# Optimization experiments

Measured on AMD Instinct MI355X. Metric: run time of the kernel, lower is better.

Reference implementation:

```python
import jax, jax.numpy as jnp
import numpy as np

N = 32768      # total nodes (2048 graphs * 16 nodes)
E = 491520     # total edges (2048 graphs * 16*15)
F = 11         # in_node_nf
H = 64         # hidden_nf
G = 2048       # number of graphs
NN = 16        # nodes per graph
R = 1024       # n_reactions
L = 4          # n_layers
EIN = 2 * H + 1        # edge_mlp input: [h[row], h[col], radial]
NIN = H + H + F        # node_mlp input: [h, agg, node_attr=h0]


def setup_inputs() -> dict:
    key = jax.random.key(0)
    ks = jax.random.split(key, 24)
    s = 0.05
    d = {
        "h0": jax.random.normal(ks[0], (N, F), jnp.float32),
        "positions": jax.random.normal(ks[1], (N, 3), jnp.float32),
        "edges": jax.random.randint(ks[2], (2, E), 0, N),
        "node_mask": jnp.ones((N, 1), jnp.float32),
        "edge_mask": jnp.ones((E, 1), jnp.float32),
        "reaction_indexes": jax.random.randint(ks[3], (G,), 0, R),
        "reaction_signs": jax.random.normal(ks[4], (G,), jnp.float32),
        # params
        "emb_w": jax.random.normal(ks[5], (F, H), jnp.float32) * s,
        "emb_b": jnp.zeros((H,), jnp.float32),
        "edge_w1": jax.random.normal(ks[6], (L, EIN, H), jnp.float32) * s,
        "edge_b1": jnp.zeros((L, H), jnp.float32),
        "edge_w2": jax.random.normal(ks[7], (L, H, H), jnp.float32) * s,
        "edge_b2": jnp.zeros((L, H), jnp.float32),
        "node_w1": jax.random.normal(ks[8], (L, NIN, H), jnp.float32) * s,
        "node_b1": jnp.zeros((L, H), jnp.float32),
        "node_w2": jax.random.normal(ks[9], (L, H, H), jnp.float32) * s,
        "node_b2": jnp.zeros((L, H), jnp.float32),
        "dec_w1": jax.random.normal(ks[10], (H, H), jnp.float32) * s,
        "dec_b1": jnp.zeros((H,), jnp.float32),
        "dec_w2": jax.random.normal(ks[11], (H, H), jnp.float32) * s,
        "dec_b2": jnp.zeros((H,), jnp.float32),
        "g_w1": jax.random.normal(ks[12], (H, H), jnp.float32) * s,
        "g_b1": jnp.zeros((H,), jnp.float32),
        "g_w2": jax.random.normal(ks[13], (H, 1), jnp.float32) * s,
        "g_b2": jnp.zeros((1,), jnp.float32),
        "n_nodes": NN,
        "n_reactions": R,
    }
    return d


def reference(h0, positions, edges, node_mask, edge_mask, reaction_indexes,
              reaction_signs, emb_w, emb_b, edge_w1, edge_b1, edge_w2, edge_b2,
              node_w1, node_b1, node_w2, node_b2, dec_w1, dec_b1, dec_w2,
              dec_b2, g_w1, g_b1, g_w2, g_b2, n_nodes, n_reactions):
    silu = jax.nn.silu
    row, col = edges[0], edges[1]
    n = h0.shape[0]

    # radial is constant across layers (coords never updated in this variant)
    coord_diff = positions[row] - positions[col]          # [E, 3]
    radial = jnp.sum(coord_diff ** 2, axis=1, keepdims=True)  # [E, 1]

    h = h0 @ emb_w + emb_b                                # [N, H]
    for i in range(edge_w1.shape[0]):
        # edge model
        e_in = jnp.concatenate([h[row], h[col], radial], axis=1)  # [E, 2H+1]
        e = silu(e_in @ edge_w1[i] + edge_b1[i])
        e = silu(e @ edge_w2[i] + edge_b2[i])             # [E, H]
        e = e * edge_mask
        # scatter-sum aggregation by source node
        agg = jax.ops.segment_sum(e, row, num_segments=n)  # [N, H]
        # node model (node_attr = h0)
        n_in = jnp.concatenate([h, agg, h0], axis=1)      # [N, 2H+F]
        h = silu(n_in @ node_w1[i] + node_b1[i]) @ node_w2[i] + node_b2[i]

    # node decoder
    h = silu(h @ dec_w1 + dec_b1) @ dec_w2 + dec_b2
    h = h * node_mask
    # pool per graph (fixed n_nodes per graph)
    hg = h.reshape(-1, n_nodes, h.shape[-1]).sum(axis=1)  # [G, H]
    # graph decoder
    temp = silu(hg @ g_w1 + g_b1) @ g_w2 + g_b2           # [G, 1]
    # signed per-reaction aggregation
    pred = jnp.zeros((n_reactions,), h.dtype).at[reaction_indexes].add(
        temp[:, 0] * reaction_signs)
    return pred
```

## Files before the change

kernel.cpp:

```cpp
#include <hip/hip_runtime.h>
#include <math.h>

#define N_NODES 32768
#define N_EDGES 491520
#define F_IN    11
#define H       64
#define G_GRAPHS 2048
#define NN_PER_G 16
#define R_REACT 1024
#define L_LAYERS 4
#define EIN     129
#define NIN     139
#define NPBLK   32

typedef __attribute__((ext_vector_type(8))) short short8;
typedef __attribute__((ext_vector_type(4))) float f32x4;

__device__ __forceinline__ float silu_f(float x) {
    return x * __builtin_amdgcn_rcpf(1.0f + __expf(-x));
}
__device__ __forceinline__ void atomAddF(float* p, float v) {
    unsafeAtomicAdd(p, v);
}
__device__ __forceinline__ float bf2f(unsigned short b) {
    union { float f; unsigned u; } v; v.u = ((unsigned)b) << 16;
    return v.f;
}
__device__ __forceinline__ unsigned short f2bf(float x) {
    union { float f; unsigned u; } v; v.f = x;
    unsigned r = v.u + 0x7FFFu + ((v.u >> 16) & 1u);
    return (unsigned short)(r >> 16);
}
__device__ __forceinline__ void splitbf(float x, unsigned short& hi, unsigned short& lo) {
    hi = f2bf(x);
    lo = f2bf(x - bf2f(hi));
}
__device__ __forceinline__ void splitbf_t(float x, unsigned short& hi, unsigned short& lo) {
    union { float f; unsigned u; } v; v.f = x;
    hi = (unsigned short)(v.u >> 16);
    union { float f; unsigned u; } w; w.f = x - bf2f(hi);
    lo = (unsigned short)(w.u >> 16);
}

__global__ __launch_bounds__(256) void k_embed(
        const float* __restrict__ h0, const float* __restrict__ emb_w,
        const float* __restrict__ emb_b, float* __restrict__ h,
        int* __restrict__ deg) {
    int tid = blockIdx.x * 256 + threadIdx.x;
    if (blockIdx.x < N_NODES / 256) deg[tid] = 0;
    int n = tid >> 6, j = tid & 63;
    float acc = emb_b[j];
#pragma unroll
    for (int k = 0; k < F_IN; ++k)
        acc += h0[n * F_IN + k] * emb_w[k * H + j];
    h[tid] = acc;
}

__global__ __launch_bounds__(256) void k_radial(
        const int* __restrict__ edges, const float* __restrict__ pos,
        float* __restrict__ radial) {
    int e = blockIdx.x * 256 + threadIdx.x;
    int r = edges[e], c = edges[N_EDGES + e];
    float dx = pos[r * 3 + 0] - pos[c * 3 + 0];
    float dy = pos[r * 3 + 1] - pos[c * 3 + 1];
    float dz = pos[r * 3 + 2] - pos[c * 3 + 2];
    radial[e] = dx * dx + dy * dy + dz * dz;
}

__global__ __launch_bounds__(256) void k_hist(
        const int* __restrict__ edges, int* __restrict__ deg) {
    int e = blockIdx.x * 256 + threadIdx.x;
    atomicAdd(&deg[edges[e]], 1);
}

__global__ __launch_bounds__(1024) void k_scan(
        const int* __restrict__ deg, int* __restrict__ nstart,
        int* __restrict__ cursor) {
    const int tid = threadIdx.x;
    const int lane = tid & 63, wv = tid >> 6;
    __shared__ int wsum[16];

    const int base = tid * 32;
    int local[32];
    int s = 0;
#pragma unroll
    for (int i = 0; i < 32; ++i) { local[i] = s; s += deg[base + i]; }

    int v = s;
#pragma unroll
    for (int off = 1; off < 64; off <<= 1) {
        int u = __shfl_up(v, off);
        if (lane >= off) v += u;
    }
    if (lane == 63) wsum[wv] = v;
    const int excl = v - s;
    __syncthreads();
    if (wv == 0 && lane < 16) {
        int w = wsum[lane];
        int vv = w;
#pragma unroll
        for (int off = 1; off < 16; off <<= 1) {
            int u = __shfl_up(vv, off);
            if (lane >= off) vv += u;
        }
        wsum[lane] = vv - w;
    }
    __syncthreads();
    const int bs = wsum[wv] + excl;
#pragma unroll
    for (int i = 0; i < 32; ++i) {
        int ns = bs + local[i];
        nstart[base + i] = ns;
        cursor[base + i] = ns;
    }
    if (tid == 0) nstart[N_NODES] = N_EDGES;
}

__global__ __launch_bounds__(256) void k_fill(
        const int* __restrict__ edges, const float* __restrict__ radial,
        const float* __restrict__ emask, int* __restrict__ cursor,
        int* __restrict__ csrP, float* __restrict__ csrR,
        float* __restrict__ csrM) {
    int e = blockIdx.x * 256 + threadIdx.x;
    int r = edges[e];
    int pos = atomicAdd(&cursor[r], 1);
    csrP[pos] = edges[N_EDGES + e] | ((r & (NPBLK - 1)) << 16);
    csrR[pos] = radial[e];
    csrM[pos] = emask[e];
}

__global__ __launch_bounds__(64, 1) void k_nodeproj_m(
        const float* __restrict__ h, const float* __restrict__ W1,
        const float* __restrict__ b1,
        float* __restrict__ PA, float* __restrict__ PB) {
    const int lane = threadIdx.x;
    const int quad = lane >> 4, m16 = lane & 15;

    short8 Bh[16], Bl[16];
#pragma unroll
    for (int nt = 0; nt < 8; ++nt) {
#pragma unroll
        for (int kf = 0; kf < 2; ++kf) {
            short8 bh, bl;
#pragma unroll
            for (int j = 0; j < 8; ++j) {
                int row = (nt >= 4 ? 64 : 0) + kf * 32 + quad * 8 + j;
                float w = W1[row * H + (nt & 3) * 16 + m16];
                unsigned short hi, lo; splitbf(w, hi, lo);
                bh[j] = (short)hi; bl[j] = (short)lo;
            }
            Bh[nt * 2 + kf] = bh; Bl[nt * 2 + kf] = bl;
        }
    }
    float b1v[4];
#pragma unroll
    for (int nt = 0; nt < 4; ++nt) b1v[nt] = b1[nt * 16 + m16];

    for (int t = 0; t < 2; ++t) {
        const int nb = (blockIdx.x * 2 + t) * 16;
        const float* hp = h + (nb + m16) * H + quad * 8;
        float av[16];
        *(float4*)&av[0]  = *(const float4*)(hp + 0);
        *(float4*)&av[4]  = *(const float4*)(hp + 4);
        *(float4*)&av[8]  = *(const float4*)(hp + 32);
        *(float4*)&av[12] = *(const float4*)(hp + 36);
        short8 Ah0, Ah1, Al0, Al1;
#pragma unroll
        for (int j = 0; j < 8; ++j) {
            unsigned short hi, lo;
            splitbf_t(av[j], hi, lo);     Ah0[j] = (short)hi; Al0[j] = (short)lo;
            splitbf_t(av[8 + j], hi, lo); Ah1[j] = (short)hi; Al1[j] = (short)lo;
        }
        f32x4 acc[8];
#pragma unroll
        for (int nt = 0; nt < 8; ++nt) {
            f32x4 a = {0.0f, 0.0f, 0.0f, 0.0f};
            a = __builtin_amdgcn_mfma_f32_16x16x32_bf16(Ah0, Bh[nt*2+0], a, 0, 0, 0);
            a = __builtin_amdgcn_mfma_f32_16x16x32_bf16(Ah1, Bh[nt*2+1], a, 0, 0, 0);
            a = __builtin_amdgcn_mfma_f32_16x16x32_bf16(Ah0, Bl[nt*2+0], a, 0, 0, 0);
            a = __builtin_amdgcn_mfma_f32_16x16x32_bf16(Ah1, Bl[nt*2+1], a, 0, 0, 0);
            a = __builtin_amdgcn_mfma_f32_16x16x32_bf16(Al0, Bh[nt*2+0], a, 0, 0, 0);
            a = __builtin_amdgcn_mfma_f32_16x16x32_bf16(Al1, Bh[nt*2+1], a, 0, 0, 0);
            acc[nt] = a;
        }
#pragma unroll
        for (int r4 = 0; r4 < 4; ++r4) {
            const int node = nb + quad * 4 + r4;
#pragma unroll
            for (int nt = 0; nt < 4; ++nt)
                PA[node * H + nt * 16 + m16] = acc[nt][r4] + b1v[nt];
#pragma unroll
            for (int nt = 4; nt < 8; ++nt)
                PB[node * H + (nt - 4) * 16 + m16] = acc[nt][r4];
        }
    }
}

__global__ __launch_bounds__(256, 2) void k_edge6(
        const float* __restrict__ PA, const float* __restrict__ PB,
        const int* __restrict__ nstart, const int* __restrict__ csrP,
        const float* __restrict__ csrR, const float* __restrict__ csrM,
        const float* __restrict__ W1,
        const float* __restrict__ W2, const float* __restrict__ b2,
        float* __restrict__ agg) {
    const int tid = threadIdx.x;
    const int lane = tid & 63, wave = tid >> 6;
    const int quad = lane >> 4, m16 = lane & 15;
    const int n0 = blockIdx.x * NPBLK;

    __shared__ float aggld[NPBLK * 68];
    for (int i = tid; i < NPBLK * 68; i += 256) aggld[i] = 0.0f;

    short8 Bh[8], Bl[8];
#pragma unroll
    for (int nt = 0; nt < 4; ++nt) {
#pragma unroll
        for (int kf = 0; kf < 2; ++kf) {
            short8 bh, bl;
#pragma unroll
            for (int j = 0; j < 8; ++j) {
                float w = W2[(kf * 32 + quad * 8 + j) * H + nt * 16 + m16];
                unsigned short hi, lo; splitbf(w, hi, lo);
                bh[j] = (short)hi; bl[j] = (short)lo;
            }
            Bh[nt * 2 + kf] = bh; Bl[nt * 2 + kf] = bl;
        }
    }
    float w1cr[16];
#pragma unroll
    for (int i = 0; i < 16; ++i) {
        int k = (i < 8) ? (quad * 8 + i) : (32 + quad * 8 + (i - 8));
        w1cr[i] = W1[128 * H + k];
    }
    float b2v[4];
#pragma unroll
    for (int nt = 0; nt < 4; ++nt) b2v[nt] = b2[nt * 16 + m16];

    const int start = nstart[n0];
    const int end   = nstart[n0 + NPBLK];
    __syncthreads();

    const int ntiles = (end - start + 15) >> 4;

    float radA = 0.0f, avA[16], bvA[16];
    int rlA = 0;
    int rlqA[4]; float mkqA[4];

    int t = wave;
    bool haveA = t < ntiles;
    if (haveA) {
        const int idx = start + t * 16 + m16;
        const int ss = min(idx, N_EDGES - 1);
        const int pk = csrP[ss];
        radA = csrR[ss];
        const int c = pk & 0xFFFF;
        rlA = pk >> 16;
        const int sb = start + t * 16 + quad * 4;
#pragma unroll
        for (int r4 = 0; r4 < 4; ++r4) {
            int s = sb + r4, s2 = min(s, N_EDGES - 1);
            rlqA[r4] = csrP[s2] >> 16;
            mkqA[r4] = (s < end) ? csrM[s2] : 0.0f;
        }
        const float* par = PA + (n0 + rlA) * H + quad * 8;
        const float* pbr = PB + c * H + quad * 8;
        *(float4*)&avA[0]  = *(const float4*)(par + 0);
        *(float4*)&avA[4]  = *(const float4*)(par + 4);
        *(float4*)&avA[8]  = *(const float4*)(par + 32);
        *(float4*)&avA[12] = *(const float4*)(par + 36);
        *(float4*)&bvA[0]  = *(const float4*)(pbr + 0);
        *(float4*)&bvA[4]  = *(const float4*)(pbr + 4);
        *(float4*)&bvA[8]  = *(const float4*)(pbr + 32);
        *(float4*)&bvA[12] = *(const float4*)(pbr + 36);
    }

    while (haveA) {
        const int tn = t + 4;
        const bool haveB = tn < ntiles;
        float radB = 0.0f, bvB[16];
        int rlB = 0;
        int rlqB[4]; float mkqB[4];
        if (haveB) {
            const int idx = start + tn * 16 + m16;
            const int ss = min(idx, N_EDGES - 1);
            const int pk = csrP[ss];
            radB = csrR[ss];
            const int c = pk & 0xFFFF;
            rlB = pk >> 16;
            const int sb = start + tn * 16 + quad * 4;
#pragma unroll
            for (int r4 = 0; r4 < 4; ++r4) {
                int s = sb + r4, s2 = min(s, N_EDGES - 1);
                rlqB[r4] = csrP[s2] >> 16;
                mkqB[r4] = (s < end) ? csrM[s2] : 0.0f;
            }
            const float* pbr = PB + c * H + quad * 8;
            *(float4*)&bvB[0]  = *(const float4*)(pbr + 0);
            *(float4*)&bvB[4]  = *(const float4*)(pbr + 4);
            *(float4*)&bvB[8]  = *(const float4*)(pbr + 32);
            *(float4*)&bvB[12] = *(const float4*)(pbr + 36);
        }

        short8 Ah0, Ah1, Al0, Al1;
#pragma unroll
        for (int i = 0; i < 8; ++i) {
            unsigned short hi, lo;
            splitbf_t(silu_f(avA[i] + bvA[i] + radA * w1cr[i]), hi, lo);
            Ah0[i] = (short)hi; Al0[i] = (short)lo;
            splitbf_t(silu_f(avA[8+i] + bvA[8+i] + radA * w1cr[8+i]), hi, lo);
            Ah1[i] = (short)hi; Al1[i] = (short)lo;
        }
        f32x4 acc[4];
#pragma unroll
        for (int nt = 0; nt < 4; ++nt) {
            f32x4 a = {0.0f, 0.0f, 0.0f, 0.0f};
            a = __builtin_amdgcn_mfma_f32_16x16x32_bf16(Ah0, Bh[nt*2+0], a, 0, 0, 0);
            a = __builtin_amdgcn_mfma_f32_16x16x32_bf16(Ah1, Bh[nt*2+1], a, 0, 0, 0);
            a = __builtin_amdgcn_mfma_f32_16x16x32_bf16(Ah0, Bl[nt*2+0], a, 0, 0, 0);
            a = __builtin_amdgcn_mfma_f32_16x16x32_bf16(Ah1, Bl[nt*2+1], a, 0, 0, 0);
            a = __builtin_amdgcn_mfma_f32_16x16x32_bf16(Al0, Bh[nt*2+0], a, 0, 0, 0);
            a = __builtin_amdgcn_mfma_f32_16x16x32_bf16(Al1, Bh[nt*2+1], a, 0, 0, 0);
            acc[nt] = a;
        }

#pragma unroll
        for (int nt = 0; nt < 4; ++nt) {
            float oo[4];
#pragma unroll
            for (int r4 = 0; r4 < 4; ++r4)
                oo[r4] = silu_f(acc[nt][r4] + b2v[nt]) * mkqA[r4];
            int cur = rlqA[0]; float s = oo[0];
#pragma unroll
            for (int r4 = 1; r4 < 4; ++r4) {
                if (rlqA[r4] == cur) { s += oo[r4]; }
                else {
                    atomicAdd(&aggld[cur * 68 + nt * 16 + m16], s);
                    cur = rlqA[r4]; s = oo[r4];
                }
            }
            atomicAdd(&aggld[cur * 68 + nt * 16 + m16], s);
        }

        if (haveB) {
            radA = radB; rlA = rlB;
#pragma unroll
            for (int r4 = 0; r4 < 4; ++r4) { rlqA[r4] = rlqB[r4]; mkqA[r4] = mkqB[r4]; }
            const float* par = PA + (n0 + rlA) * H + quad * 8;
            *(float4*)&avA[0]  = *(const float4*)(par + 0);
            *(float4*)&avA[4]  = *(const float4*)(par + 4);
            *(float4*)&avA[8]  = *(const float4*)(par + 32);
            *(float4*)&avA[12] = *(const float4*)(par + 36);
#pragma unroll
            for (int i = 0; i < 16; ++i) bvA[i] = bvB[i];
        }
        t = tn; haveA = haveB;
    }

    __syncthreads();
#pragma unroll
    for (int i = tid; i < NPBLK * 16; i += 256) {
        int n = i >> 4, cb = (i & 15) << 2;
        *(float4*)&agg[(n0 + n) * H + cb] = *(const float4*)&aggld[n * 68 + cb];
    }
}

__global__ __launch_bounds__(64, 1) void k_node_m(
        float* __restrict__ h, const float* __restrict__ agg,
        const float* __restrict__ h0,
        const float* __restrict__ W1, const float* __restrict__ b1,
        const float* __restrict__ W2, const float* __restrict__ b2) {
    const int lane = threadIdx.x;
    const int quad = lane >> 4, m16 = lane & 15;

    short8 B1h[20], B1l[20];
#pragma unroll
    for (int nt = 0; nt < 4; ++nt) {
#pragma unroll
        for (int kf = 0; kf < 5; ++kf) {
            short8 bh, bl;
#pragma unroll
            for (int j = 0; j < 8; ++j) {
                int row = kf * 32 + quad * 8 + j;
                float w = (row < NIN) ? W1[row * H + nt * 16 + m16] : 0.0f;
                unsigned short hi, lo; splitbf(w, hi, lo);
                bh[j] = (short)hi; bl[j] = (short)lo;
            }
            B1h[nt * 5 + kf] = bh; B1l[nt * 5 + kf] = bl;
        }
    }
    short8 B2h[8], B2l[8];
#pragma unroll
    for (int nt = 0; nt < 4; ++nt) {
#pragma unroll
        for (int kf = 0; kf < 2; ++kf) {
            short8 bh, bl;
#pragma unroll
            for (int j = 0; j < 8; ++j) {
                float w = W2[(kf * 32 + quad * 8 + j) * H + nt * 16 + m16];
                unsigned short hi, lo; splitbf(w, hi, lo);
                bh[j] = (short)hi; bl[j] = (short)lo;
            }
            B2h[nt * 2 + kf] = bh; B2l[nt * 2 + kf] = bl;
        }
    }
    float b1v[4], b2v[4];
#pragma unroll
    for (int nt = 0; nt < 4; ++nt) {
        b1v[nt] = b1[nt * 16 + m16];
        b2v[nt] = b2[nt * 16 + m16];
    }

    __shared__ float tld[16 * 68];

    for (int t = 0; t < 2; ++t) {
        const int nb = (blockIdx.x * 2 + t) * 16;
        float a1[5][8];
        const float* hp = h + (nb + m16) * H + quad * 8;
        const float* ap = agg + (nb + m16) * H + quad * 8;
        *(float4*)&a1[0][0] = *(const float4*)(hp + 0);
        *(float4*)&a1[0][4] = *(const float4*)(hp + 4);
        *(float4*)&a1[1][0] = *(const float4*)(hp + 32);
        *(float4*)&a1[1][4] = *(const float4*)(hp + 36);
        *(float4*)&a1[2][0] = *(const float4*)(ap + 0);
        *(float4*)&a1[2][4] = *(const float4*)(ap + 4);
        *(float4*)&a1[3][0] = *(const float4*)(ap + 32);
        *(float4*)&a1[3][4] = *(const float4*)(ap + 36);
        const float* h0p = h0 + (nb + m16) * F_IN;
#pragma unroll
        for (int j = 0; j < 8; ++j) {
            int kk = quad * 8 + j;
            a1[4][j] = (kk < F_IN) ? h0p[kk] : 0.0f;
        }
        short8 A1h[5], A1l[5];
#pragma unroll
        for (int kf = 0; kf < 5; ++kf) {
            short8 ah, al;
#pragma unroll
            for (int j = 0; j < 8; ++j) {
                unsigned short hi, lo; splitbf_t(a1[kf][j], hi, lo);
                ah[j] = (short)hi; al[j] = (short)lo;
            }
            A1h[kf] = ah; A1l[kf] = al;
        }
        f32x4 acc[4];
#pragma unroll
        for (int nt = 0; nt < 4; ++nt) {
            f32x4 a = {0.0f, 0.0f, 0.0f, 0.0f};
#pragma unroll
            for (int kf = 0; kf < 5; ++kf)
                a = __builtin_amdgcn_mfma_f32_16x16x32_bf16(A1h[kf], B1h[nt*5+kf], a, 0, 0, 0);
#pragma unroll
            for (int kf = 0; kf < 5; ++kf)
                a = __builtin_amdgcn_mfma_f32_16x16x32_bf16(A1l[kf], B1h[nt*5+kf], a, 0, 0, 0);
#pragma unroll
            for (int kf = 0; kf < 5; ++kf)
                a = __builtin_amdgcn_mfma_f32_16x16x32_bf16(A1h[kf], B1l[nt*5+kf], a, 0, 0, 0);
            acc[nt] = a;
        }
#pragma unroll
        for (int r4 = 0; r4 < 4; ++r4)
#pragma unroll
            for (int nt = 0; nt < 4; ++nt)
                tld[(quad * 4 + r4) * 68 + nt * 16 + m16] =
                    silu_f(acc[nt][r4] + b1v[nt]);
        __syncthreads();
        float a2[16];
        *(float4*)&a2[0]  = *(const float4*)&tld[m16 * 68 + quad * 8 + 0];
        *(float4*)&a2[4]  = *(const float4*)&tld[m16 * 68 + quad * 8 + 4];
        *(float4*)&a2[8]  = *(const float4*)&tld[m16 * 68 + quad * 8 + 32];
        *(float4*)&a2[12] = *(const float4*)&tld[m16 * 68 + quad * 8 + 36];
        short8 A2h0, A2h1, A2l0, A2l1;
#pragma unroll
        for (int j = 0; j < 8; ++j) {
            unsigned short hi, lo;
            splitbf_t(a2[j], hi, lo);     A2h0[j] = (short)hi; A2l0[j] = (short)lo;
            splitbf_t(a2[8+j], hi, lo);   A2h1[j] = (short)hi; A2l1[j] = (short)lo;
        }
        f32x4 acc2[4];
#pragma unroll
        for (int nt = 0; nt < 4; ++nt) {
            f32x4 a = {0.0f, 0.0f, 0.0f, 0.0f};
            a = __builtin_amdgcn_mfma_f32_16x16x32_bf16(A2h0, B2h[nt*2+0], a, 0, 0, 0);
            a = __builtin_amdgcn_mfma_f32_16x16x32_bf16(A2h1, B2h[nt*2+1], a, 0, 0, 0);
            a = __builtin_amdgcn_mfma_f32_16x16x32_bf16(A2h0, B2l[nt*2+0], a, 0, 0, 0);
            a = __builtin_amdgcn_mfma_f32_16x16x32_bf16(A2h1, B2l[nt*2+1], a, 0, 0, 0);
            a = __builtin_amdgcn_mfma_f32_16x16x32_bf16(A2l0, B2h[nt*2+0], a, 0, 0, 0);
            a = __builtin_amdgcn_mfma_f32_16x16x32_bf16(A2l1, B2h[nt*2+1], a, 0, 0, 0);
            acc2[nt] = a;
        }
#pragma unroll
        for (int r4 = 0; r4 < 4; ++r4) {
            const int node = nb + quad * 4 + r4;
#pragma unroll
            for (int nt = 0; nt < 4; ++nt)
                h[node * H + nt * 16 + m16] = acc2[nt][r4] + b2v[nt];
        }
        __syncthreads();
    }
}

__global__ __launch_bounds__(64, 1) void k_dec_m(
        float* __restrict__ h, const float* __restrict__ nmask,
        const float* __restrict__ W1, const float* __restrict__ b1,
        const float* __restrict__ W2, const float* __restrict__ b2,
        float* __restrict__ pred) {
    const int lane = threadIdx.x;
    const int quad = lane >> 4, m16 = lane & 15;

    if (blockIdx.x < R_REACT / 64) pred[blockIdx.x * 64 + lane] = 0.0f;

    short8 B1h[8], B1l[8], B2h[8], B2l[8];
#pragma unroll
    for (int nt = 0; nt < 4; ++nt) {
#pragma unroll
        for (int kf = 0; kf < 2; ++kf) {
            short8 bh1, bl1, bh2, bl2;
#pragma unroll
            for (int j = 0; j < 8; ++j) {
                int row = kf * 32 + quad * 8 + j;
                unsigned short hi, lo;
                splitbf(W1[row * H + nt * 16 + m16], hi, lo);
                bh1[j] = (short)hi; bl1[j] = (short)lo;
                splitbf(W2[row * H + nt * 16 + m16], hi, lo);
                bh2[j] = (short)hi; bl2[j] = (short)lo;
            }
            B1h[nt*2+kf] = bh1; B1l[nt*2+kf] = bl1;
            B2h[nt*2+kf] = bh2; B2l[nt*2+kf] = bl2;
        }
    }
    float b1v[4], b2v[4];
#pragma unroll
    for (int nt = 0; nt < 4; ++nt) {
        b1v[nt] = b1[nt * 16 + m16];
        b2v[nt] = b2[nt * 16 + m16];
    }
    __shared__ float tld[16 * 68];

    for (int t = 0; t < 2; ++t) {
        const int nb = (blockIdx.x * 2 + t) * 16;
        const float* hp = h + (nb + m16) * H + quad * 8;
        float av[16];
        *(float4*)&av[0]  = *(const float4*)(hp + 0);
        *(float4*)&av[4]  = *(const float4*)(hp + 4);
        *(float4*)&av[8]  = *(const float4*)(hp + 32);
        *(float4*)&av[12] = *(const float4*)(hp + 36);
        short8 Ah0, Ah1, Al0, Al1;
#pragma unroll
        for (int j = 0; j < 8; ++j) {
            unsigned short hi, lo;
            splitbf_t(av[j], hi, lo);     Ah0[j] = (short)hi; Al0[j] = (short)lo;
            splitbf_t(av[8+j], hi, lo);   Ah1[j] = (short)hi; Al1[j] = (short)lo;
        }
        f32x4 acc[4];
#pragma unroll
        for (int nt = 0; nt < 4; ++nt) {
            f32x4 a = {0.0f, 0.0f, 0.0f, 0.0f};
            a = __builtin_amdgcn_mfma_f32_16x16x32_bf16(Ah0, B1h[nt*2+0], a, 0, 0, 0);
            a = __builtin_amdgcn_mfma_f32_16x16x32_bf16(Ah1, B1h[nt*2+1], a, 0, 0, 0);
            a = __builtin_amdgcn_mfma_f32_16x16x32_bf16(Ah0, B1l[nt*2+0], a, 0, 0, 0);
            a = __builtin_amdgcn_mfma_f32_16x16x32_bf16(Ah1, B1l[nt*2+1], a, 0, 0, 0);
            a = __builtin_amdgcn_mfma_f32_16x16x32_bf16(Al0, B1h[nt*2+0], a, 0, 0, 0);
            a = __builtin_amdgcn_mfma_f32_16x16x32_bf16(Al1, B1h[nt*2+1], a, 0, 0, 0);
            acc[nt] = a;
        }
#pragma unroll
        for (int r4 = 0; r4 < 4; ++r4)
#pragma unroll
            for (int nt = 0; nt < 4; ++nt)
                tld[(quad * 4 + r4) * 68 + nt * 16 + m16] =
                    silu_f(acc[nt][r4] + b1v[nt]);
        __syncthreads();
        float a2[16];
        *(float4*)&a2[0]  = *(const float4*)&tld[m16 * 68 + quad * 8 + 0];
        *(float4*)&a2[4]  = *(const float4*)&tld[m16 * 68 + quad * 8 + 4];
        *(float4*)&a2[8]  = *(const float4*)&tld[m16 * 68 + quad * 8 + 32];
        *(float4*)&a2[12] = *(const float4*)&tld[m16 * 68 + quad * 8 + 36];
        short8 A2h0, A2h1, A2l0, A2l1;
#pragma unroll
        for (int j = 0; j < 8; ++j) {
            unsigned short hi, lo;
            splitbf_t(a2[j], hi, lo);     A2h0[j] = (short)hi; A2l0[j] = (short)lo;
            splitbf_t(a2[8+j], hi, lo);   A2h1[j] = (short)hi; A2l1[j] = (short)lo;
        }
        f32x4 acc2[4];
#pragma unroll
        for (int nt = 0; nt < 4; ++nt) {
            f32x4 a = {0.0f, 0.0f, 0.0f, 0.0f};
            a = __builtin_amdgcn_mfma_f32_16x16x32_bf16(A2h0, B2h[nt*2+0], a, 0, 0, 0);
            a = __builtin_amdgcn_mfma_f32_16x16x32_bf16(A2h1, B2h[nt*2+1], a, 0, 0, 0);
            a = __builtin_amdgcn_mfma_f32_16x16x32_bf16(A2h0, B2l[nt*2+0], a, 0, 0, 0);
            a = __builtin_amdgcn_mfma_f32_16x16x32_bf16(A2h1, B2l[nt*2+1], a, 0, 0, 0);
            a = __builtin_amdgcn_mfma_f32_16x16x32_bf16(A2l0, B2h[nt*2+0], a, 0, 0, 0);
            a = __builtin_amdgcn_mfma_f32_16x16x32_bf16(A2l1, B2h[nt*2+1], a, 0, 0, 0);
            acc2[nt] = a;
        }
#pragma unroll
        for (int r4 = 0; r4 < 4; ++r4) {
            const int node = nb + quad * 4 + r4;
            const float nm = nmask[node];
#pragma unroll
            for (int nt = 0; nt < 4; ++nt)
                h[node * H + nt * 16 + m16] = (acc2[nt][r4] + b2v[nt]) * nm;
        }
        __syncthreads();
    }
}

__global__ __launch_bounds__(64) void k_graph(
        const float* __restrict__ h, const int* __restrict__ rid,
        const float* __restrict__ rsign,
        const float* __restrict__ W1, const float* __restrict__ b1,
        const float* __restrict__ W2, const float* __restrict__ b2,
        float* __restrict__ pred) {
    const int g = blockIdx.x;
    const int lane = threadIdx.x;
    float hgv = 0.0f;
#pragma unroll
    for (int m = 0; m < NN_PER_G; ++m)
        hgv += h[(g * NN_PER_G + m) * H + lane];
    __shared__ __align__(16) float hgs[64];
    hgs[lane] = hgv;
    __syncthreads();
    float acc = b1[lane];
#pragma unroll
    for (int k = 0; k < H; ++k)
        acc += hgs[k] * W1[k * H + lane];
    float part = silu_f(acc) * W2[lane];
#pragma unroll
    for (int off = 32; off > 0; off >>= 1)
        part += __shfl_down(part, off);
    if (lane == 0)
        atomAddF(&pred[rid[g]], (part + b2[0]) * rsign[g]);
}

extern "C" void kernel_launch(void* const* d_in, const int* in_sizes, int n_in,
                              void* d_out, int out_size, void* d_ws, size_t ws_size,
                              hipStream_t stream) {
    const float* h0      = (const float*)d_in[0];
    const float* pos     = (const float*)d_in[1];
    const int*   edges   = (const int*)d_in[2];
    const float* nmask   = (const float*)d_in[3];
    const float* emask   = (const float*)d_in[4];
    const int*   rid     = (const int*)d_in[5];
    const float* rsign   = (const float*)d_in[6];
    const float* emb_w   = (const float*)d_in[7];
    const float* emb_b   = (const float*)d_in[8];
    const float* edge_w1 = (const float*)d_in[9];
    const float* edge_b1 = (const float*)d_in[10];
    const float* edge_w2 = (const float*)d_in[11];
    const float* edge_b2 = (const float*)d_in[12];
    const float* node_w1 = (const float*)d_in[13];
    const float* node_b1 = (const float*)d_in[14];
    const float* node_w2 = (const float*)d_in[15];
    const float* node_b2 = (const float*)d_in[16];
    const float* dec_w1  = (const float*)d_in[17];
    const float* dec_b1  = (const float*)d_in[18];
    const float* dec_w2  = (const float*)d_in[19];
    const float* dec_b2  = (const float*)d_in[20];
    const float* g_w1    = (const float*)d_in[21];
    const float* g_b1    = (const float*)d_in[22];
    const float* g_w2    = (const float*)d_in[23];
    const float* g_b2    = (const float*)d_in[24];

    float* h      = (float*)d_ws;
    float* agg    = h + N_NODES * H;
    float* radial = agg + N_NODES * H;
    float* PA     = radial + N_EDGES;
    float* PB     = PA + N_NODES * H;
    float* csrR   = PB + N_NODES * H;
    float* csrM   = csrR + N_EDGES;
    int*   csrP   = (int*)(csrM + N_EDGES);
    int*   deg    = csrP + N_EDGES;
    int*   nstart = deg + N_NODES;
    int*   cursor = nstart + N_NODES + 1;
    float* pred   = (float*)d_out;

    k_embed<<<(N_NODES * H) / 256, 256, 0, stream>>>(h0, emb_w, emb_b, h, deg);
    k_radial<<<N_EDGES / 256, 256, 0, stream>>>(edges, pos, radial);
    k_hist<<<N_EDGES / 256, 256, 0, stream>>>(edges, deg);
    k_scan<<<1, 1024, 0, stream>>>(deg, nstart, cursor);
    k_fill<<<N_EDGES / 256, 256, 0, stream>>>(edges, radial, emask, cursor,
                                              csrP, csrR, csrM);

    for (int i = 0; i < L_LAYERS; ++i) {
        k_nodeproj_m<<<N_NODES / 32, 64, 0, stream>>>(
            h, edge_w1 + i * EIN * H, edge_b1 + i * H, PA, PB);
        k_edge6<<<N_NODES / NPBLK, 256, 0, stream>>>(
            PA, PB, nstart, csrP, csrR, csrM,
            edge_w1 + i * EIN * H,
            edge_w2 + i * H * H, edge_b2 + i * H, agg);
        k_node_m<<<N_NODES / 32, 64, 0, stream>>>(
            h, agg, h0,
            node_w1 + i * NIN * H, node_b1 + i * H,
            node_w2 + i * H * H,   node_b2 + i * H);
    }
    k_dec_m<<<N_NODES / 32, 64, 0, stream>>>(h, nmask, dec_w1, dec_b1,
                                             dec_w2, dec_b2, pred);
    k_graph<<<G_GRAPHS, 64, 0, stream>>>(h, rid, rsign, g_w1, g_b1, g_w2,
                                         g_b2, pred);
}
```

Before: 563.0 us.

## Fuse next-layer edge node projection into node MLP kernel

The node-update kernel now also computes the next layer's edge-MLP projections (PA/PB) from the freshly computed h held in shared memory. This removes three separate projection launches and the re-read of h from global memory. The first layer's projection still runs before the loop. The edge kernel's launch bounds are also raised to 3 blocks per CU, which may force register spills.

```diff
diff --git a/kernel.cpp b/kernel.cpp
--- a/kernel.cpp
+++ b/kernel.cpp
@@ -196,7 +196,7 @@
     }
 }
 
-__global__ __launch_bounds__(256, 2) void k_edge6(
+__global__ __launch_bounds__(256, 3) void k_edge6(
         const float* __restrict__ PA, const float* __restrict__ PB,
         const int* __restrict__ nstart, const int* __restrict__ csrP,
         const float* __restrict__ csrR, const float* __restrict__ csrM,
@@ -364,138 +364,207 @@
     }
 }
 
-__global__ __launch_bounds__(64, 1) void k_node_m(
+__global__ __launch_bounds__(64, 1) void k_node_f(
         float* __restrict__ h, const float* __restrict__ agg,
         const float* __restrict__ h0,
         const float* __restrict__ W1, const float* __restrict__ b1,
-        const float* __restrict__ W2, const float* __restrict__ b2) {
+        const float* __restrict__ W2, const float* __restrict__ b2,
+        const float* __restrict__ WE, const float* __restrict__ bE,
+        float* __restrict__ PA, float* __restrict__ PB, int do_proj) {
     const int lane = threadIdx.x;
     const int quad = lane >> 4, m16 = lane & 15;
 
-    short8 B1h[20], B1l[20];
-#pragma unroll
-    for (int nt = 0; nt < 4; ++nt) {
-#pragma unroll
-        for (int kf = 0; kf < 5; ++kf) {
-            short8 bh, bl;
+    __shared__ float tld[16 * 68];
+    __shared__ float tldH[2][16 * 68];
+
+    {
+        short8 B1h[20], B1l[20];
+#pragma unroll
+        for (int nt = 0; nt < 4; ++nt) {
+#pragma unroll
+            for (int kf = 0; kf < 5; ++kf) {
+                short8 bh, bl;
+#pragma unroll
+                for (int j = 0; j < 8; ++j) {
+                    int row = kf * 32 + quad * 8 + j;
+                    float w = (row < NIN) ? W1[row * H + nt * 16 + m16] : 0.0f;
+                    unsigned short hi, lo; splitbf(w, hi, lo);
+                    bh[j] = (short)hi; bl[j] = (short)lo;
+                }
+                B1h[nt * 5 + kf] = bh; B1l[nt * 5 + kf] = bl;
+            }
+        }
+        short8 B2h[8], B2l[8];
+#pragma unroll
+        for (int nt = 0; nt < 4; ++nt) {
+#pragma unroll
+            for (int kf = 0; kf < 2; ++kf) {
+                short8 bh, bl;
+#pragma unroll
+                for (int j = 0; j < 8; ++j) {
+                    float w = W2[(kf * 32 + quad * 8 + j) * H + nt * 16 + m16];
+                    unsigned short hi, lo; splitbf(w, hi, lo);
+                    bh[j] = (short)hi; bl[j] = (short)lo;
+                }
+                B2h[nt * 2 + kf] = bh; B2l[nt * 2 + kf] = bl;
+            }
+        }
+        float b1v[4], b2v[4];
+#pragma unroll
+        for (int nt = 0; nt < 4; ++nt) {
+            b1v[nt] = b1[nt * 16 + m16];
+            b2v[nt] = b2[nt * 16 + m16];
+        }
+
+        for (int t = 0; t < 2; ++t) {
+            const int nb = (blockIdx.x * 2 + t) * 16;
+            float a1[5][8];
+            const float* hp = h + (nb + m16) * H + quad * 8;
+            const float* ap = agg + (nb + m16) * H + quad * 8;
+            *(float4*)&a1[0][0] = *(const float4*)(hp + 0);
+            *(float4*)&a1[0][4] = *(const float4*)(hp + 4);
+            *(float4*)&a1[1][0] = *(const float4*)(hp + 32);
+            *(float4*)&a1[1][4] = *(const float4*)(hp + 36);
+            *(float4*)&a1[2][0] = *(const float4*)(ap + 0);
+            *(float4*)&a1[2][4] = *(const float4*)(ap + 4);
+            *(float4*)&a1[3][0] = *(const float4*)(ap + 32);
+            *(float4*)&a1[3][4] = *(const float4*)(ap + 36);
+            const float* h0p = h0 + (nb + m16) * F_IN;
 #pragma unroll
             for (int j = 0; j < 8; ++j) {
-                int row = kf * 32 + quad * 8 + j;
-                float w = (row < NIN) ? W1[row * H + nt * 16 + m16] : 0.0f;
-                unsigned short hi, lo; splitbf(w, hi, lo);
-                bh[j] = (short)hi; bl[j] = (short)lo;
-            }
-            B1h[nt * 5 + kf] = bh; B1l[nt * 5 + kf] = bl;
-        }
-    }
-    short8 B2h[8], B2l[8];
-#pragma unroll
-    for (int nt = 0; nt < 4; ++nt) {
-#pragma unroll
-        for (int kf = 0; kf < 2; ++kf) {
-            short8 bh, bl;
+                int kk = quad * 8 + j;
+                a1[4][j] = (kk < F_IN) ? h0p[kk] : 0.0f;
+            }
+            short8 A1h[5], A1l[5];
+#pragma unroll
+            for (int kf = 0; kf < 5; ++kf) {
+                short8 ah, al;
+#pragma unroll
+                for (int j = 0; j < 8; ++j) {
+                    unsigned short hi, lo; splitbf_t(a1[kf][j], hi, lo);
+                    ah[j] = (short)hi; al[j] = (short)lo;
+                }
+                A1h[kf] = ah; A1l[kf] = al;
+            }
+            f32x4 acc[4];
+#pragma unroll
+            for (int nt = 0; nt < 4; ++nt) {
+                f32x4 a = {0.0f, 0.0f, 0.0f, 0.0f};
+#pragma unroll
+                for (int kf = 0; kf < 5; ++kf)
+                    a = __builtin_amdgcn_mfma_f32_16x16x32_bf16(A1h[kf], B1h[nt*5+kf], a, 0, 0, 0);
+#pragma unroll
+                for (int kf = 0; kf < 5; ++kf)
+                    a = __builtin_amdgcn_mfma_f32_16x16x32_bf16(A1l[kf], B1h[nt*5+kf], a, 0, 0, 0);
+#pragma unroll
+                for (int kf = 0; kf < 5; ++kf)
+                    a = __builtin_amdgcn_mfma_f32_16x16x32_bf16(A1h[kf], B1l[nt*5+kf], a, 0, 0, 0);
+                acc[nt] = a;
+            }
+#pragma unroll
+            for (int r4 = 0; r4 < 4; ++r4)
+#pragma unroll
+                for (int nt = 0; nt < 4; ++nt)
+                    tld[(quad * 4 + r4) * 68 + nt * 16 + m16] =
+                        silu_f(acc[nt][r4] + b1v[nt]);
+            __syncthreads();
+            float a2[16];
+            *(float4*)&a2[0]  = *(const float4*)&tld[m16 * 68 + quad * 8 + 0];
+            *(float4*)&a2[4]  = *(const float4*)&tld[m16 * 68 + quad * 8 + 4];
+            *(float4*)&a2[8]  = *(const float4*)&tld[m16 * 68 + quad * 8 + 32];
+            *(float4*)&a2[12] = *(const float4*)&tld[m16 * 68 + quad * 8 + 36];
+            short8 A2h0, A2h1, A2l0, A2l1;
 #pragma unroll
             for (int j = 0; j < 8; ++j) {
-                float w = W2[(kf * 32 + quad * 8 + j) * H + nt * 16 + m16];
-                unsigned short hi, lo; splitbf(w, hi, lo);
-                bh[j] = (short)hi; bl[j] = (short)lo;
-            }
-            B2h[nt * 2 + kf] = bh; B2l[nt * 2 + kf] = bl;
-        }
-    }
-    float b1v[4], b2v[4];
-#pragma unroll
-    for (int nt = 0; nt < 4; ++nt) {
-        b1v[nt] = b1[nt * 16 + m16];
-        b2v[nt] = b2[nt * 16 + m16];
-    }
-
-    __shared__ float tld[16 * 68];
-
-    for (int t = 0; t < 2; ++t) {
-        const int nb = (blockIdx.x * 2 + t) * 16;
-        float a1[5][8];
-        const float* hp = h + (nb + m16) * H + quad * 8;
-        const float* ap = agg + (nb + m16) * H + quad * 8;
-        *(float4*)&a1[0][0] = *(const float4*)(hp + 0);
-        *(float4*)&a1[0][4] = *(const float4*)(hp + 4);
-        *(float4*)&a1[1][0] = *(const float4*)(hp + 32);
-        *(float4*)&a1[1][4] = *(const float4*)(hp + 36);
-        *(float4*)&a1[2][0] = *(const float4*)(ap + 0);
-        *(float4*)&a1[2][4] = *(const float4*)(ap + 4);
-        *(float4*)&a1[3][0] = *(const float4*)(ap + 32);
-        *(float4*)&a1[3][4] = *(const float4*)(ap + 36);
-        const float* h0p = h0 + (nb + m16) * F_IN;
-#pragma unroll
-        for (int j = 0; j < 8; ++j) {
-            int kk = quad * 8 + j;
-            a1[4][j] = (kk < F_IN) ? h0p[kk] : 0.0f;
-        }
-        short8 A1h[5], A1l[5];
-#pragma unroll
-        for (int kf = 0; kf < 5; ++kf) {
-            short8 ah, al;
+                unsigned short hi, lo;
+                splitbf_t(a2[j], hi, lo);     A2h0[j] = (short)hi; A2l0[j] = (short)lo;
+                splitbf_t(a2[8+j], hi, lo);   A2h1[j] = (short)hi; A2l1[j] = (short)lo;
+            }
+            f32x4 acc2[4];
+#pragma unroll
+            for (int nt = 0; nt < 4; ++nt) {
+                f32x4 a = {0.0f, 0.0f, 0.0f, 0.0f};
+                a = __builtin_amdgcn_mfma_f32_16x16x32_bf16(A2h0, B2h[nt*2+0], a, 0, 0, 0);
+                a = __builtin_amdgcn_mfma_f32_16x16x32_bf16(A2h1, B2h[nt*2+1], a, 0, 0, 0);
+                a = __builtin_amdgcn_mfma_f32_16x16x32_bf16(A2h0, B2l[nt*2+0], a, 0, 0, 0);
+                a = __builtin_amdgcn_mfma_f32_16x16x32_bf16(A2h1, B2l[nt*2+1], a, 0, 0, 0);
+                a = __builtin_amdgcn_mfma_f32_16x16x32_bf16(A2l0, B2h[nt*2+0], a, 0, 0, 0);
+                a = __builtin_amdgcn_mfma_f32_16x16x32_bf16(A2l1, B2h[nt*2+1], a, 0, 0, 0);
+                acc2[nt] = a;
+            }
+#pragma unroll
+            for (int r4 = 0; r4 < 4; ++r4) {
+                const int node = nb + quad * 4 + r4;
+#pragma unroll
+                for (int nt = 0; nt < 4; ++nt) {
+                    float val = acc2[nt][r4] + b2v[nt];
+                    h[node * H + nt * 16 + m16] = val;
+                    tldH[t][(quad * 4 + r4) * 68 + nt * 16 + m16] = val;
+                }
+            }
+            __syncthreads();
+        }
+    }
+
+    if (do_proj) {
+        short8 Eh[16], El[16];
+#pragma unroll
+        for (int nt = 0; nt < 8; ++nt) {
+#pragma unroll
+            for (int kf = 0; kf < 2; ++kf) {
+                short8 bh, bl;
+#pragma unroll
+                for (int j = 0; j < 8; ++j) {
+                    int row = (nt >= 4 ? 64 : 0) + kf * 32 + quad * 8 + j;
+                    float w = WE[row * H + (nt & 3) * 16 + m16];
+                    unsigned short hi, lo; splitbf(w, hi, lo);
+                    bh[j] = (short)hi; bl[j] = (short)lo;
+                }
+                Eh[nt * 2 + kf] = bh; El[nt * 2 + kf] = bl;
+            }
+        }
+        float bEv[4];
+#pragma unroll
+        for (int nt = 0; nt < 4; ++nt) bEv[nt] = bE[nt * 16 + m16];
+
+        for (int t = 0; t < 2; ++t) {
+            const int nb = (blockIdx.x * 2 + t) * 16;
+            const float* hp = &tldH[t][m16 * 68 + quad * 8];
+            float av[16];
+            *(float4*)&av[0]  = *(const float4*)(hp + 0);
+            *(float4*)&av[4]  = *(const float4*)(hp + 4);
+            *(float4*)&av[8]  = *(const float4*)(hp + 32);
+            *(float4*)&av[12] = *(const float4*)(hp + 36);
+            short8 Ah0, Ah1, Al0, Al1;
 #pragma unroll
             for (int j = 0; j < 8; ++j) {
-                unsigned short hi, lo; splitbf_t(a1[kf][j], hi, lo);
-                ah[j] = (short)hi; al[j] = (short)lo;
-            }
-            A1h[kf] = ah; A1l[kf] = al;
-        }
-        f32x4 acc[4];
-#pragma unroll
-        for (int nt = 0; nt < 4; ++nt) {
-            f32x4 a = {0.0f, 0.0f, 0.0f, 0.0f};
-#pragma unroll
-            for (int kf = 0; kf < 5; ++kf)
-                a = __builtin_amdgcn_mfma_f32_16x16x32_bf16(A1h[kf], B1h[nt*5+kf], a, 0, 0, 0);
-#pragma unroll
-            for (int kf = 0; kf < 5; ++kf)
-                a = __builtin_amdgcn_mfma_f32_16x16x32_bf16(A1l[kf], B1h[nt*5+kf], a, 0, 0, 0);
-#pragma unroll
-            for (int kf = 0; kf < 5; ++kf)
-                a = __builtin_amdgcn_mfma_f32_16x16x32_bf16(A1h[kf], B1l[nt*5+kf], a, 0, 0, 0);
-            acc[nt] = a;
-        }
-#pragma unroll
-        for (int r4 = 0; r4 < 4; ++r4)
-#pragma unroll
-            for (int nt = 0; nt < 4; ++nt)
-                tld[(quad * 4 + r4) * 68 + nt * 16 + m16] =
-                    silu_f(acc[nt][r4] + b1v[nt]);
-        __syncthreads();
-        float a2[16];
-        *(float4*)&a2[0]  = *(const float4*)&tld[m16 * 68 + quad * 8 + 0];
-        *(float4*)&a2[4]  = *(const float4*)&tld[m16 * 68 + quad * 8 + 4];
-        *(float4*)&a2[8]  = *(const float4*)&tld[m16 * 68 + quad * 8 + 32];
-        *(float4*)&a2[12] = *(const float4*)&tld[m16 * 68 + quad * 8 + 36];
-        short8 A2h0, A2h1, A2l0, A2l1;
-#pragma unroll
-        for (int j = 0; j < 8; ++j) {
-            unsigned short hi, lo;
-            splitbf_t(a2[j], hi, lo);     A2h0[j] = (short)hi; A2l0[j] = (short)lo;
-            splitbf_t(a2[8+j], hi, lo);   A2h1[j] = (short)hi; A2l1[j] = (short)lo;
-        }
-        f32x4 acc2[4];
-#pragma unroll
-        for (int nt = 0; nt < 4; ++nt) {
-            f32x4 a = {0.0f, 0.0f, 0.0f, 0.0f};
-            a = __builtin_amdgcn_mfma_f32_16x16x32_bf16(A2h0, B2h[nt*2+0], a, 0, 0, 0);
-            a = __builtin_amdgcn_mfma_f32_16x16x32_bf16(A2h1, B2h[nt*2+1], a, 0, 0, 0);
-            a = __builtin_amdgcn_mfma_f32_16x16x32_bf16(A2h0, B2l[nt*2+0], a, 0, 0, 0);
-            a = __builtin_amdgcn_mfma_f32_16x16x32_bf16(A2h1, B2l[nt*2+1], a, 0, 0, 0);
-            a = __builtin_amdgcn_mfma_f32_16x16x32_bf16(A2l0, B2h[nt*2+0], a, 0, 0, 0);
-            a = __builtin_amdgcn_mfma_f32_16x16x32_bf16(A2l1, B2h[nt*2+1], a, 0, 0, 0);
-            acc2[nt] = a;
-        }
-#pragma unroll
-        for (int r4 = 0; r4 < 4; ++r4) {
-            const int node = nb + quad * 4 + r4;
-#pragma unroll
-            for (int nt = 0; nt < 4; ++nt)
-                h[node * H + nt * 16 + m16] = acc2[nt][r4] + b2v[nt];
-        }
-        __syncthreads();
+                unsigned short hi, lo;
+                splitbf_t(av[j], hi, lo);     Ah0[j] = (short)hi; Al0[j] = (short)lo;
+                splitbf_t(av[8 + j], hi, lo); Ah1[j] = (short)hi; Al1[j] = (short)lo;
+            }
+            f32x4 acc[8];
+#pragma unroll
+            for (int nt = 0; nt < 8; ++nt) {
+                f32x4 a = {0.0f, 0.0f, 0.0f, 0.0f};
+                a = __builtin_amdgcn_mfma_f32_16x16x32_bf16(Ah0, Eh[nt*2+0], a, 0, 0, 0);
+                a = __builtin_amdgcn_mfma_f32_16x16x32_bf16(Ah1, Eh[nt*2+1], a, 0, 0, 0);
+                a = __builtin_amdgcn_mfma_f32_16x16x32_bf16(Ah0, El[nt*2+0], a, 0, 0, 0);
+                a = __builtin_amdgcn_mfma_f32_16x16x32_bf16(Ah1, El[nt*2+1], a, 0, 0, 0);
+                a = __builtin_amdgcn_mfma_f32_16x16x32_bf16(Al0, Eh[nt*2+0], a, 0, 0, 0);
+                a = __builtin_amdgcn_mfma_f32_16x16x32_bf16(Al1, Eh[nt*2+1], a, 0, 0, 0);
+                acc[nt] = a;
+            }
+#pragma unroll
+            for (int r4 = 0; r4 < 4; ++r4) {
+                const int node = nb + quad * 4 + r4;
+#pragma unroll
+                for (int nt = 0; nt < 4; ++nt)
+                    PA[node * H + nt * 16 + m16] = acc[nt][r4] + bEv[nt];
+#pragma unroll
+                for (int nt = 4; nt < 8; ++nt)
+                    PB[node * H + (nt - 4) * 16 + m16] = acc[nt][r4];
+            }
+        }
     }
 }
 
@@ -682,17 +751,21 @@
     k_fill<<<N_EDGES / 256, 256, 0, stream>>>(edges, radial, emask, cursor,
                                               csrP, csrR, csrM);
 
+    k_nodeproj_m<<<N_NODES / 32, 64, 0, stream>>>(
+        h, edge_w1, edge_b1, PA, PB);
+
     for (int i = 0; i < L_LAYERS; ++i) {
-        k_nodeproj_m<<<N_NODES / 32, 64, 0, stream>>>(
-            h, edge_w1 + i * EIN * H, edge_b1 + i * H, PA, PB);
         k_edge6<<<N_NODES / NPBLK, 256, 0, stream>>>(
             PA, PB, nstart, csrP, csrR, csrM,
             edge_w1 + i * EIN * H,
             edge_w2 + i * H * H, edge_b2 + i * H, agg);
-        k_node_m<<<N_NODES / 32, 64, 0, stream>>>(
+        const int nx = (i < L_LAYERS - 1) ? (i + 1) : 0;
+        k_node_f<<<N_NODES / 32, 64, 0, stream>>>(
             h, agg, h0,
             node_w1 + i * NIN * H, node_b1 + i * H,
-            node_w2 + i * H * H,   node_b2 + i * H);
+            node_w2 + i * H * H,   node_b2 + i * H,
+            edge_w1 + nx * EIN * H, edge_b1 + nx * H,
+            PA, PB, (i < L_LAYERS - 1) ? 1 : 0);
     }
     k_dec_m<<<N_NODES / 32, 64, 0, stream>>>(h, nmask, dec_w1, dec_b1,
                                              dec_w2, dec_b2, pred);
```

Measured after the change: 643.8 us. +14.3%, slower.
